# Optimization experiments

Hardware: AMD Instinct MI355X
Metric: run time of the kernel (lower is better)

The kernel has to match this reference:

```python
import jax, jax.numpy as jnp
import numpy as np

NUM_CLASSES = 1000
B, Q, N = 64, 900, 30
NO_OBJ_W = 0.1
COST_CLASS, COST_BBOX, COST_GIOU = 1.0, 5.0, 2.0
LOSS_BBOX, LOSS_GIOU = 5.0, 2.0


def cxcywh_to_xyxy(b):
    cx, cy, w, h = b[..., 0], b[..., 1], b[..., 2], b[..., 3]
    return jnp.stack([cx - 0.5 * w, cy - 0.5 * h, cx + 0.5 * w, cy + 0.5 * h], axis=-1)


def _area(b):
    return jnp.clip(b[..., 2] - b[..., 0], 0.0) * jnp.clip(b[..., 3] - b[..., 1], 0.0)


def giou_xyxy(b1, b2):
    # GIoU over broadcastable [..., 4] xyxy boxes
    lt = jnp.maximum(b1[..., :2], b2[..., :2])
    rb = jnp.minimum(b1[..., 2:], b2[..., 2:])
    wh = jnp.clip(rb - lt, 0.0)
    inter = wh[..., 0] * wh[..., 1]
    union = _area(b1) + _area(b2) - inter
    iou = inter / jnp.maximum(union, 1e-6)
    ltc = jnp.minimum(b1[..., :2], b2[..., :2])
    rbc = jnp.maximum(b1[..., 2:], b2[..., 2:])
    whc = jnp.clip(rbc - ltc, 0.0)
    ac = whc[..., 0] * whc[..., 1]
    return iou - (ac - union) / jnp.maximum(ac, 1e-6)


def _cost_matrices(pred_logits, pred_boxes, tgt_labels, tgt_boxes_xyxy):
    prob = jax.nn.softmax(pred_logits, axis=-1)                    # [B,Q,C+1]
    cost_cls = -jax.vmap(lambda p, l: p[:, l])(prob, tgt_labels)   # [B,Q,N]
    pred_xyxy = jnp.clip(cxcywh_to_xyxy(pred_boxes), 0.0, 1.0)     # [B,Q,4]
    cost_l1 = jnp.sum(jnp.abs(pred_xyxy[:, :, None] - tgt_boxes_xyxy[:, None]), -1)
    cost_g = -giou_xyxy(pred_xyxy[:, :, None], tgt_boxes_xyxy[:, None])
    C = COST_CLASS * cost_cls + COST_BBOX * cost_l1 + COST_GIOU * cost_g
    return C, pred_xyxy


def greedy_match(C):
    # faithful to the module's torch fallback matcher: iteratively pick the
    # global minimum of the cost matrix, masking used rows/cols (host-side,
    # non-differentiable, exactly like the detach->cpu->assignment in torch)
    Cw = C.copy()
    Qn, Nn = Cw.shape
    rows, cols = [], []
    for _ in range(min(Qn, Nn)):
        i = int(np.argmin(Cw))
        pi, ti = divmod(i, Nn)
        rows.append(pi)
        cols.append(ti)
        Cw[pi, :] = 1e9
        Cw[:, ti] = 1e9
    return np.array(rows, dtype=np.int32), np.array(cols, dtype=np.int32)


def match_all(Cnp):
    pis, tis = zip(*[greedy_match(Cnp[b]) for b in range(Cnp.shape[0])])
    return jnp.asarray(np.stack(pis)), jnp.asarray(np.stack(tis))  # [B,N] each


def set_losses(pred_logits, pred_xyxy, tgt_labels, tgt_boxes_xyxy, pi, ti):
    ce_weight = jnp.ones(NUM_CLASSES + 1, jnp.float32).at[NUM_CLASSES].set(NO_OBJ_W)
    bidx = jnp.arange(B)[:, None]
    # target class per query: matched -> tgt label, else no-object class
    tc = jnp.full((B, Q), NUM_CLASSES, dtype=jnp.int32)
    tc = tc.at[bidx, pi].set(jnp.take_along_axis(tgt_labels, ti, axis=1))
    nll = -jnp.take_along_axis(jax.nn.log_softmax(pred_logits, -1), tc[..., None].astype(jnp.int32), axis=2)[..., 0]
    w = ce_weight[tc]
    ce = jnp.mean(jnp.sum(w * nll, axis=1) / jnp.sum(w, axis=1))  # torch weighted CE mean, per image
    p_m = pred_xyxy[bidx, pi]          # [B,N,4] matched preds
    t_m = tgt_boxes_xyxy[bidx, ti]     # [B,N,4] matched targets
    l1 = jnp.mean(jnp.mean(jnp.abs(p_m - t_m), axis=(1, 2)))
    gl = jnp.mean(jnp.mean(1.0 - giou_xyxy(p_m, t_m), axis=1))
    total = ce + LOSS_BBOX * l1 + LOSS_GIOU * gl
    return jnp.stack([total, ce, l1, gl])


def setup_inputs():
    key = jax.random.key(0)
    k1, k2, k3, k4, k5 = jax.random.split(key, 5)
    pred_logits = jax.random.normal(k1, (B, Q, NUM_CLASSES + 1), jnp.float32)
    pred_boxes = jax.random.uniform(k2, (B, Q, 4), jnp.float32, 0.05, 0.95)
    tgt_labels = jax.random.randint(k3, (B, N), 0, NUM_CLASSES, dtype=jnp.int32)
    lt = jax.random.uniform(k4, (B, N, 2), jnp.float32, 0.0, 0.6)
    wh = jax.random.uniform(k5, (B, N, 2), jnp.float32, 0.02, 0.37)
    tgt_boxes_xyxy = jnp.concatenate([lt, lt + wh], axis=-1)  # valid 0..1 xyxy
    return {"pred_logits": pred_logits, "pred_boxes": pred_boxes,
            "tgt_labels": tgt_labels, "tgt_boxes_xyxy": tgt_boxes_xyxy}


def reference(pred_logits, pred_boxes, tgt_labels, tgt_boxes_xyxy):
    C, pred_xyxy = _cost_matrices(pred_logits, pred_boxes, tgt_labels, tgt_boxes_xyxy)
    pi, ti = match_all(np.asarray(jax.lax.stop_gradient(C)))
    # returns [loss_total, loss_ce, loss_bbox, loss_giou]
    return set_losses(pred_logits, pred_xyxy, tgt_labels, tgt_boxes_xyxy, pi, ti)
```

## Files before the change

### kernel.cpp

```cpp
#include <hip/hip_runtime.h>
#include <math.h>

#define BB 64
#define QQ 900
#define NN 30
#define C1 1001
#define QN (QQ * NN)
#define NO_OBJ_W 0.1f

__device__ unsigned g_ord[BB * QN];
__device__ unsigned long long g_top[BB * NN * NN];
__device__ float  g_logZ[BB * QQ];
__device__ float  g_noobj[BB * QQ];
__device__ float4 g_xyxy[BB * QQ];
__device__ int    g_pi[BB * NN];
__device__ int    g_ti[BB * NN];
__device__ float4 g_partial[BB];

__device__ __forceinline__ float giou_f(float ax1, float ay1, float ax2, float ay2,
                                        float bx1, float by1, float bx2, float by2) {
    float ix1 = fmaxf(ax1, bx1), iy1 = fmaxf(ay1, by1);
    float ix2 = fminf(ax2, bx2), iy2 = fminf(ay2, by2);
    float iw = fmaxf(ix2 - ix1, 0.f), ih = fmaxf(iy2 - iy1, 0.f);
    float inter = iw * ih;
    float areaA = fmaxf(ax2 - ax1, 0.f) * fmaxf(ay2 - ay1, 0.f);
    float areaB = fmaxf(bx2 - bx1, 0.f) * fmaxf(by2 - by1, 0.f);
    float uni = areaA + areaB - inter;
    float iou = inter / fmaxf(uni, 1e-6f);
    float cx1 = fminf(ax1, bx1), cy1 = fminf(ay1, by1);
    float cx2 = fmaxf(ax2, bx2), cy2 = fmaxf(ay2, by2);
    float cw = fmaxf(cx2 - cx1, 0.f), ch = fmaxf(cy2 - cy1, 0.f);
    float ac = cw * ch;
    return iou - (ac - uni) / fmaxf(ac, 1e-6f);
}

__device__ __forceinline__ unsigned ord_map(float f) {
    unsigned u = __float_as_uint(f);
    return (u & 0x80000000u) ? ~u : (u | 0x80000000u);
}

__global__ __launch_bounds__(256) void cost_kernel(const float* __restrict__ logits,
                                                   const float* __restrict__ pboxes,
                                                   const int*   __restrict__ labels,
                                                   const float* __restrict__ tboxes) {
    int gwave = (blockIdx.x * blockDim.x + threadIdx.x) >> 6;
    int lane = threadIdx.x & 63;
    if (gwave >= BB * QQ) return;
    int b = gwave / QQ;

    size_t s = (size_t)gwave * C1;
    size_t a0 = (s + 3) >> 2;
    size_t a1 = (s + C1) >> 2;
    int nq = (int)(a1 - a0);
    int hh = (int)(a0 * 4 - s);
    int tt = (int)((s + C1) - a1 * 4);
    const float4* L4 = (const float4*)logits;

    float4 v4[4];
#pragma unroll
    for (int i = 0; i < 4; ++i) {
        int qq = lane + 64 * i;
        v4[i] = (qq < nq) ? L4[a0 + qq]
                          : make_float4(-INFINITY, -INFINITY, -INFINITY, -INFINITY);
    }
    float e1 = (lane < hh) ? logits[s + lane] : -INFINITY;
    float e2 = (lane < tt) ? logits[a1 * 4 + lane] : -INFINITY;

    float mx = fmaxf(e1, e2);
#pragma unroll
    for (int i = 0; i < 4; ++i)
        mx = fmaxf(mx, fmaxf(fmaxf(v4[i].x, v4[i].y), fmaxf(v4[i].z, v4[i].w)));
#pragma unroll
    for (int off = 32; off; off >>= 1) mx = fmaxf(mx, __shfl_xor(mx, off));

    float sm = __expf(e1 - mx) + __expf(e2 - mx);
#pragma unroll
    for (int i = 0; i < 4; ++i) {
        sm += __expf(v4[i].x - mx);
        sm += __expf(v4[i].y - mx);
        sm += __expf(v4[i].z - mx);
        sm += __expf(v4[i].w - mx);
    }
#pragma unroll
    for (int off = 32; off; off >>= 1) sm += __shfl_xor(sm, off);
    float logZ = mx + __logf(sm);

    float row1000 = logits[s + 1000];

    const float* pb = pboxes + (size_t)gwave * 4;
    float cx = pb[0], cy = pb[1], w = pb[2], h = pb[3];
    float x1 = fminf(fmaxf(cx - 0.5f * w, 0.f), 1.f);
    float y1 = fminf(fmaxf(cy - 0.5f * h, 0.f), 1.f);
    float x2 = fminf(fmaxf(cx + 0.5f * w, 0.f), 1.f);
    float y2 = fminf(fmaxf(cy + 0.5f * h, 0.f), 1.f);

    if (lane == 0) {
        g_logZ[gwave] = logZ;
        g_noobj[gwave] = logZ - row1000;
        g_xyxy[gwave] = make_float4(x1, y1, x2, y2);
    }

    if (lane < NN) {
        int t = lane;
        int lab = labels[b * NN + t];
        float pcls = __expf(logits[s + lab] - logZ);
        const float* tb = tboxes + ((size_t)(b * NN + t)) * 4;
        float tx1 = tb[0], ty1 = tb[1], tx2 = tb[2], ty2 = tb[3];
        float l1 = fabsf(x1 - tx1) + fabsf(y1 - ty1) + fabsf(x2 - tx2) + fabsf(y2 - ty2);
        float g = giou_f(x1, y1, x2, y2, tx1, ty1, tx2, ty2);
        g_ord[(size_t)gwave * NN + t] = ord_map(-pcls + 5.0f * l1 - 2.0f * g);
    }
}

__global__ __launch_bounds__(256) void select_kernel() {
    int gw = (blockIdx.x * blockDim.x + threadIdx.x) >> 6;
    int lane = threadIdx.x & 63;
    int wid = (threadIdx.x >> 6) & 3;
    if (gw >= BB * NN) return;
    int b = gw / NN;
    int t = gw - b * NN;

    __shared__ unsigned long long s_ls[4][960];

    unsigned long long key[16];
    if (lane < 60) {
#pragma unroll
        for (int j = 0; j < 15; ++j) {
            int q = j * 60 + lane;
            unsigned o = g_ord[((size_t)(b * QQ + q)) * NN + t];
            key[j] = ((unsigned long long)o << 32) | (unsigned)(q * NN + t);
        }
    } else {
#pragma unroll
        for (int j = 0; j < 15; ++j) key[j] = ~0ull;
    }
    key[15] = ~0ull;

#pragma unroll
    for (int kk = 2; kk <= 16; kk <<= 1) {
#pragma unroll
        for (int jj = kk >> 1; jj > 0; jj >>= 1) {
#pragma unroll
            for (int i = 0; i < 16; ++i) {
                int l = i ^ jj;
                if (l > i) {
                    bool up = ((i & kk) == 0);
                    unsigned long long a = key[i], c = key[l];
                    bool sw = up ? (a > c) : (a < c);
                    key[i] = sw ? c : a;
                    key[l] = sw ? a : c;
                }
            }
        }
    }

#pragma unroll
    for (int j = 0; j < 15; ++j) s_ls[wid][j * 64 + lane] = key[j];

    unsigned long long h = key[0];
    int p = 0;
    unsigned long long* outp = g_top + (size_t)gw * NN;
    for (int it = 0; it < NN; ++it) {
        unsigned long long m = h;
#pragma unroll
        for (int off = 32; off; off >>= 1) {
            unsigned long long o = __shfl_xor(m, off);
            m = (o < m) ? o : m;
        }
        if (lane == it) outp[it] = m;
        if (h == m) {
            ++p;
            h = (p < 15) ? s_ls[wid][p * 64 + lane] : ~0ull;
        }
    }
}

__global__ __launch_bounds__(64) void match_kernel() {
    int b = blockIdx.x;
    int lane = threadIdx.x;

    __shared__ unsigned long long s_cand[NN * NN];
    __shared__ unsigned s_dead[29];

    const unsigned long long* topb = g_top + (size_t)b * NN * NN;
#pragma unroll
    for (int k = 0; k < 15; ++k) {
        int i = lane + 64 * k;
        if (i < NN * NN) s_cand[i] = topb[i];
    }
    if (lane < 29) s_dead[lane] = 0u;

    bool colLive = lane < NN;
    int ptr = 0;
    unsigned long long cand = colLive ? s_cand[lane * NN] : ~0ull;
    unsigned rowc = colLive ? ((unsigned)cand) / NN : 0u;

    for (int it = 0; it < NN; ++it) {
        unsigned long long g = colLive ? cand : ~0ull;
#pragma unroll
        for (int off = 32; off; off >>= 1) {
            unsigned long long o = __shfl_xor(g, off);
            g = (o < g) ? o : g;
        }
        unsigned e = (unsigned)g;
        int pq = e / NN;
        int pt = e - pq * NN;
        if (lane == 0) {
            g_pi[b * NN + it] = pq;
            g_ti[b * NN + it] = pt;
            s_dead[pq >> 5] |= (1u << (pq & 31));
        }
        if (lane == pt) colLive = false;
        if (colLive && rowc == (unsigned)pq) {
            do {
                ++ptr;
                cand = s_cand[lane * NN + ptr];
                rowc = ((unsigned)cand) / NN;
            } while ((s_dead[rowc >> 5] >> (rowc & 31)) & 1u);
        }
    }
}

__global__ __launch_bounds__(256) void loss_kernel(const float* __restrict__ logits,
                                                   const int*   __restrict__ labels,
                                                   const float* __restrict__ tboxes) {
    int b = blockIdx.x;
    int tid = threadIdx.x;

    float sA = 0.f;
    for (int q = tid; q < QQ; q += 256) sA += g_noobj[b * QQ + q];

    float sB = 0.f, sL = 0.f, sG = 0.f;
    if (tid < NN) {
        int pq = g_pi[b * NN + tid], pt = g_ti[b * NN + tid];
        int gq = b * QQ + pq;
        int lab = labels[b * NN + pt];
        float mnll = g_logZ[gq] - logits[(size_t)gq * C1 + lab];
        sB = mnll - NO_OBJ_W * g_noobj[gq];
        float4 p = g_xyxy[gq];
        const float* tb = tboxes + ((size_t)(b * NN + pt)) * 4;
        float tx1 = tb[0], ty1 = tb[1], tx2 = tb[2], ty2 = tb[3];
        sL = fabsf(p.x - tx1) + fabsf(p.y - ty1) + fabsf(p.z - tx2) + fabsf(p.w - ty2);
        sG = 1.0f - giou_f(p.x, p.y, p.z, p.w, tx1, ty1, tx2, ty2);
    }

    __shared__ float s4[4][4];
    int lane = tid & 63, wid = tid >> 6;
    float vv[4] = {sA, sB, sL, sG};
#pragma unroll
    for (int j = 0; j < 4; ++j) {
        float x = vv[j];
#pragma unroll
        for (int off = 32; off; off >>= 1) x += __shfl_xor(x, off);
        if (lane == 0) s4[wid][j] = x;
    }
    __syncthreads();
    if (tid == 0) {
        float a = 0.f, bs = 0.f, l = 0.f, g = 0.f;
        for (int w = 0; w < 4; ++w) { a += s4[w][0]; bs += s4[w][1]; l += s4[w][2]; g += s4[w][3]; }
        g_partial[b] = make_float4(NO_OBJ_W * a + bs, l, g, 0.f);
    }
}

__global__ __launch_bounds__(64) void final_kernel(float* __restrict__ out) {
    int b = threadIdx.x;
    float4 p = g_partial[b];
    float ce = p.x, l1 = p.y, gl = p.z;
#pragma unroll
    for (int off = 32; off; off >>= 1) {
        ce += __shfl_xor(ce, off);
        l1 += __shfl_xor(l1, off);
        gl += __shfl_xor(gl, off);
    }
    if (b == 0) {
        ce /= (float)(BB * 117);
        l1 /= (float)(BB * NN * 4);
        gl /= (float)(BB * NN);
        out[0] = ce + 5.0f * l1 + 2.0f * gl;
        out[1] = ce;
        out[2] = l1;
        out[3] = gl;
    }
}

extern "C" void kernel_launch(void* const* d_in, const int* in_sizes, int n_in,
                              void* d_out, int out_size, void* d_ws, size_t ws_size,
                              hipStream_t stream) {
    const float* pred_logits = (const float*)d_in[0];
    const float* pred_boxes  = (const float*)d_in[1];
    const int*   tgt_labels  = (const int*)d_in[2];
    const float* tgt_boxes   = (const float*)d_in[3];
    float* out = (float*)d_out;

    cost_kernel<<<(BB * QQ) / 4, 256, 0, stream>>>(pred_logits, pred_boxes, tgt_labels, tgt_boxes);
    select_kernel<<<(BB * NN) / 4, 256, 0, stream>>>();
    match_kernel<<<BB, 64, 0, stream>>>();
    loss_kernel<<<BB, 256, 0, stream>>>(pred_logits, tgt_labels, tgt_boxes);
    final_kernel<<<1, 64, 0, stream>>>(out);
}
```

Before: 99.00 us.

## Fuse match, loss and final reduction into one kernel with atomic finalize

Merges the match, loss and final kernels into a single per-batch kernel. Matches stay in shared memory, and the last block reduces through atomics plus a completion counter, which cuts two kernel launches. The select kernel now shifts its register-held sorted keys instead of reading them back from shared memory. Logit loads use nontemporal hints. The accumulators are reset inside cost_kernel, which relies on stream ordering. The atomic float summation order is nondeterministic.

```diff
diff --git a/kernel.cpp b/kernel.cpp
--- a/kernel.cpp
+++ b/kernel.cpp
@@ -8,14 +8,15 @@
 #define QN (QQ * NN)
 #define NO_OBJ_W 0.1f
 
+typedef float f4v __attribute__((ext_vector_type(4)));
+
 __device__ unsigned g_ord[BB * QN];
 __device__ unsigned long long g_top[BB * NN * NN];
 __device__ float  g_logZ[BB * QQ];
 __device__ float  g_noobj[BB * QQ];
 __device__ float4 g_xyxy[BB * QQ];
-__device__ int    g_pi[BB * NN];
-__device__ int    g_ti[BB * NN];
-__device__ float4 g_partial[BB];
+__device__ float  g_acc[3];
+__device__ unsigned g_cnt;
 
 __device__ __forceinline__ float giou_f(float ax1, float ay1, float ax2, float ay2,
                                         float bx1, float by1, float bx2, float by2) {
@@ -43,6 +44,10 @@
                                                    const float* __restrict__ pboxes,
                                                    const int*   __restrict__ labels,
                                                    const float* __restrict__ tboxes) {
+    if (blockIdx.x == 0 && threadIdx.x == 0) {
+        g_acc[0] = 0.f; g_acc[1] = 0.f; g_acc[2] = 0.f;
+        g_cnt = 0u;
+    }
     int gwave = (blockIdx.x * blockDim.x + threadIdx.x) >> 6;
     int lane = threadIdx.x & 63;
     if (gwave >= BB * QQ) return;
@@ -54,17 +59,17 @@
     int nq = (int)(a1 - a0);
     int hh = (int)(a0 * 4 - s);
     int tt = (int)((s + C1) - a1 * 4);
-    const float4* L4 = (const float4*)logits;
-
-    float4 v4[4];
+    const f4v* L4 = (const f4v*)logits;
+
+    f4v v4[4];
 #pragma unroll
     for (int i = 0; i < 4; ++i) {
         int qq = lane + 64 * i;
-        v4[i] = (qq < nq) ? L4[a0 + qq]
-                          : make_float4(-INFINITY, -INFINITY, -INFINITY, -INFINITY);
-    }
-    float e1 = (lane < hh) ? logits[s + lane] : -INFINITY;
-    float e2 = (lane < tt) ? logits[a1 * 4 + lane] : -INFINITY;
+        if (qq < nq) v4[i] = __builtin_nontemporal_load(&L4[a0 + qq]);
+        else         v4[i] = (f4v){-INFINITY, -INFINITY, -INFINITY, -INFINITY};
+    }
+    float e1 = (lane < hh) ? __builtin_nontemporal_load(&logits[s + lane]) : -INFINITY;
+    float e2 = (lane < tt) ? __builtin_nontemporal_load(&logits[a1 * 4 + lane]) : -INFINITY;
 
     float mx = fmaxf(e1, e2);
 #pragma unroll
@@ -115,12 +120,9 @@
 __global__ __launch_bounds__(256) void select_kernel() {
     int gw = (blockIdx.x * blockDim.x + threadIdx.x) >> 6;
     int lane = threadIdx.x & 63;
-    int wid = (threadIdx.x >> 6) & 3;
     if (gw >= BB * NN) return;
     int b = gw / NN;
     int t = gw - b * NN;
-
-    __shared__ unsigned long long s_ls[4][960];
 
     unsigned long long key[16];
     if (lane < 60) {
@@ -154,85 +156,80 @@
         }
     }
 
-#pragma unroll
-    for (int j = 0; j < 15; ++j) s_ls[wid][j * 64 + lane] = key[j];
-
-    unsigned long long h = key[0];
-    int p = 0;
     unsigned long long* outp = g_top + (size_t)gw * NN;
     for (int it = 0; it < NN; ++it) {
-        unsigned long long m = h;
+        unsigned long long m = key[0];
 #pragma unroll
         for (int off = 32; off; off >>= 1) {
             unsigned long long o = __shfl_xor(m, off);
             m = (o < m) ? o : m;
         }
         if (lane == it) outp[it] = m;
-        if (h == m) {
-            ++p;
-            h = (p < 15) ? s_ls[wid][p * 64 + lane] : ~0ull;
-        }
-    }
-}
-
-__global__ __launch_bounds__(64) void match_kernel() {
-    int b = blockIdx.x;
-    int lane = threadIdx.x;
-
-    __shared__ unsigned long long s_cand[NN * NN];
-    __shared__ unsigned s_dead[29];
-
-    const unsigned long long* topb = g_top + (size_t)b * NN * NN;
-#pragma unroll
-    for (int k = 0; k < 15; ++k) {
-        int i = lane + 64 * k;
-        if (i < NN * NN) s_cand[i] = topb[i];
-    }
-    if (lane < 29) s_dead[lane] = 0u;
-
-    bool colLive = lane < NN;
-    int ptr = 0;
-    unsigned long long cand = colLive ? s_cand[lane * NN] : ~0ull;
-    unsigned rowc = colLive ? ((unsigned)cand) / NN : 0u;
-
-    for (int it = 0; it < NN; ++it) {
-        unsigned long long g = colLive ? cand : ~0ull;
-#pragma unroll
-        for (int off = 32; off; off >>= 1) {
-            unsigned long long o = __shfl_xor(g, off);
-            g = (o < g) ? o : g;
-        }
-        unsigned e = (unsigned)g;
-        int pq = e / NN;
-        int pt = e - pq * NN;
-        if (lane == 0) {
-            g_pi[b * NN + it] = pq;
-            g_ti[b * NN + it] = pt;
-            s_dead[pq >> 5] |= (1u << (pq & 31));
-        }
-        if (lane == pt) colLive = false;
-        if (colLive && rowc == (unsigned)pq) {
-            do {
-                ++ptr;
-                cand = s_cand[lane * NN + ptr];
-                rowc = ((unsigned)cand) / NN;
-            } while ((s_dead[rowc >> 5] >> (rowc & 31)) & 1u);
-        }
-    }
-}
-
-__global__ __launch_bounds__(256) void loss_kernel(const float* __restrict__ logits,
-                                                   const int*   __restrict__ labels,
-                                                   const float* __restrict__ tboxes) {
+        if (key[0] == m) {
+#pragma unroll
+            for (int j = 0; j < 15; ++j) key[j] = key[j + 1];
+            key[15] = ~0ull;
+        }
+    }
+}
+
+__global__ __launch_bounds__(256) void match_loss_kernel(const float* __restrict__ logits,
+                                                         const int*   __restrict__ labels,
+                                                         const float* __restrict__ tboxes,
+                                                         float* __restrict__ out) {
     int b = blockIdx.x;
     int tid = threadIdx.x;
 
+    __shared__ unsigned long long s_cand[NN * NN];
+    __shared__ int s_pi[NN], s_ti[NN];
+    __shared__ unsigned s_dead[29];
+    __shared__ float s4[4][4];
+
+    const unsigned long long* topb = g_top + (size_t)b * NN * NN;
+    for (int i = tid; i < NN * NN; i += 256) s_cand[i] = topb[i];
+    if (tid < 29) s_dead[tid] = 0u;
+    __syncthreads();
+
+    if (tid < 64) {
+        int lane = tid;
+        bool colLive = lane < NN;
+        int ptr = 0;
+        unsigned long long cand = colLive ? s_cand[lane * NN] : ~0ull;
+        unsigned rowc = colLive ? ((unsigned)cand) / NN : 0u;
+
+        for (int it = 0; it < NN; ++it) {
+            unsigned long long g = colLive ? cand : ~0ull;
+#pragma unroll
+            for (int off = 32; off; off >>= 1) {
+                unsigned long long o = __shfl_xor(g, off);
+                g = (o < g) ? o : g;
+            }
+            unsigned e = (unsigned)g;
+            int pq = e / NN;
+            int pt = e - pq * NN;
+            if (lane == 0) {
+                s_pi[it] = pq;
+                s_ti[it] = pt;
+                s_dead[pq >> 5] |= (1u << (pq & 31));
+            }
+            if (lane == pt) colLive = false;
+            if (colLive && rowc == (unsigned)pq) {
+                do {
+                    ++ptr;
+                    cand = s_cand[lane * NN + ptr];
+                    rowc = ((unsigned)cand) / NN;
+                } while ((s_dead[rowc >> 5] >> (rowc & 31)) & 1u);
+            }
+        }
+    }
+    __syncthreads();
+
     float sA = 0.f;
     for (int q = tid; q < QQ; q += 256) sA += g_noobj[b * QQ + q];
 
     float sB = 0.f, sL = 0.f, sG = 0.f;
     if (tid < NN) {
-        int pq = g_pi[b * NN + tid], pt = g_ti[b * NN + tid];
+        int pq = s_pi[tid], pt = s_ti[tid];
         int gq = b * QQ + pq;
         int lab = labels[b * NN + pt];
         float mnll = g_logZ[gq] - logits[(size_t)gq * C1 + lab];
@@ -244,7 +241,6 @@
         sG = 1.0f - giou_f(p.x, p.y, p.z, p.w, tx1, ty1, tx2, ty2);
     }
 
-    __shared__ float s4[4][4];
     int lane = tid & 63, wid = tid >> 6;
     float vv[4] = {sA, sB, sL, sG};
 #pragma unroll
@@ -258,28 +254,21 @@
     if (tid == 0) {
         float a = 0.f, bs = 0.f, l = 0.f, g = 0.f;
         for (int w = 0; w < 4; ++w) { a += s4[w][0]; bs += s4[w][1]; l += s4[w][2]; g += s4[w][3]; }
-        g_partial[b] = make_float4(NO_OBJ_W * a + bs, l, g, 0.f);
-    }
-}
-
-__global__ __launch_bounds__(64) void final_kernel(float* __restrict__ out) {
-    int b = threadIdx.x;
-    float4 p = g_partial[b];
-    float ce = p.x, l1 = p.y, gl = p.z;
-#pragma unroll
-    for (int off = 32; off; off >>= 1) {
-        ce += __shfl_xor(ce, off);
-        l1 += __shfl_xor(l1, off);
-        gl += __shfl_xor(gl, off);
-    }
-    if (b == 0) {
-        ce /= (float)(BB * 117);
-        l1 /= (float)(BB * NN * 4);
-        gl /= (float)(BB * NN);
-        out[0] = ce + 5.0f * l1 + 2.0f * gl;
-        out[1] = ce;
-        out[2] = l1;
-        out[3] = gl;
+        atomicAdd(&g_acc[0], NO_OBJ_W * a + bs);
+        atomicAdd(&g_acc[1], l);
+        atomicAdd(&g_acc[2], g);
+        __threadfence();
+        unsigned prev = atomicAdd(&g_cnt, 1u);
+        if (prev == BB - 1) {
+            __threadfence();
+            float ce = atomicAdd(&g_acc[0], 0.f) / (float)(BB * 117);
+            float l1 = atomicAdd(&g_acc[1], 0.f) / (float)(BB * NN * 4);
+            float gl = atomicAdd(&g_acc[2], 0.f) / (float)(BB * NN);
+            out[0] = ce + 5.0f * l1 + 2.0f * gl;
+            out[1] = ce;
+            out[2] = l1;
+            out[3] = gl;
+        }
     }
 }
 
@@ -294,7 +283,5 @@
 
     cost_kernel<<<(BB * QQ) / 4, 256, 0, stream>>>(pred_logits, pred_boxes, tgt_labels, tgt_boxes);
     select_kernel<<<(BB * NN) / 4, 256, 0, stream>>>();
-    match_kernel<<<BB, 64, 0, stream>>>();
-    loss_kernel<<<BB, 256, 0, stream>>>(pred_logits, tgt_labels, tgt_boxes);
-    final_kernel<<<1, 64, 0, stream>>>(out);
-}
+    match_loss_kernel<<<BB, 256, 0, stream>>>(pred_logits, tgt_labels, tgt_boxes, out);
+}
```

Measured after the change: 104.9 us. 6.0% more time.
